# Optimization experiments

Hardware: AMD Instinct MI355X
Metric: run time of the kernel (lower is better)

## Reference

```python
import jax, jax.numpy as jnp
import numpy as np

W = 128
POS_FREQ = 10  # -> 3*10*2 = 60 encoded dims
VIEW_FREQ = 4  # -> 3*4*2 = 24 encoded dims


def freq_encode(v, n_freq):
    # tcnn 'Frequency' encoding: sin/cos of 2^j * pi * x per input dim.
    scales = (2.0 ** jnp.arange(n_freq, dtype=v.dtype)) * jnp.pi  # [F]
    ang = v[..., :, None] * scales  # [N, 3, F]
    enc = jnp.stack([jnp.sin(ang), jnp.cos(ang)], axis=-1)  # [N, 3, F, 2]
    return enc.reshape(v.shape[0], -1)  # [N, 3*F*2]


def mlp(h, weights):
    # tcnn FullyFusedMLP: bias-free, ReLU on hidden layers, linear output.
    for Wm in weights[:-1]:
        h = jax.nn.relu(h @ Wm)
    return h @ weights[-1]


def setup_inputs():
    key = jax.random.key(0)
    ks = jax.random.split(key, 10)
    N = 1048576

    def w(k, fan_in, fan_out):
        s = (1.0 / np.sqrt(fan_in)).astype(np.float32)
        return jax.random.uniform(k, (fan_in, fan_out), jnp.float32, -s, s)

    return {
        "x": jax.random.uniform(ks[0], (N, 6), jnp.float32),
        "Wd1_0": w(ks[1], 60, W),
        "Wd1_1": w(ks[2], W, W),
        "Wd1_2": w(ks[3], W, W),
        "Wd2_0": w(ks[4], 60 + W, W),
        "Wd2_1": w(ks[5], W, W),
        "Wd2_2": w(ks[6], W, W),
        "Wd2_3": w(ks[7], W, W + 1),
        "Wc_0": w(ks[8], 24 + W, W),
        "Wc_1": w(ks[9], W, 3),
    }


def reference(x, Wd1_0, Wd1_1, Wd1_2, Wd2_0, Wd2_1, Wd2_2, Wd2_3, Wc_0, Wc_1):
    pos, view = x[:, :3], x[:, 3:6]
    # Density MLP
    enc_pos = freq_encode(pos, POS_FREQ)                # [N, 60]
    part1 = mlp(enc_pos, [Wd1_0, Wd1_1, Wd1_2])          # [N, 128]
    dens_out = mlp(jnp.concatenate([enc_pos, part1], -1),
                   [Wd2_0, Wd2_1, Wd2_2, Wd2_3])         # [N, 129]
    blending = jax.nn.sigmoid(dens_out[:, :1])           # [N, 1]
    feature = dens_out[:, 1:]                            # [N, 128]
    density = feature[:, 0:1]                            # [N, 1]
    # Color MLP
    enc_view = freq_encode(view, VIEW_FREQ)              # [N, 24]
    rgb = mlp(jnp.concatenate([enc_view, feature], -1), [Wc_0, Wc_1])  # [N, 3]
    return jnp.concatenate([rgb, density, blending], -1)  # [N, 5]
```

## Files before the change

kernel.cpp:

```cpp
#include <hip/hip_runtime.h>
#include <cstdint>
#include <cstddef>

typedef __attribute__((ext_vector_type(8))) __bf16 bf16x8;
typedef __attribute__((ext_vector_type(16))) float floatx16;

struct SrcPtrs { const float* p[9]; };


__global__ void prep_zero(unsigned short* __restrict__ ws) {
  uint4* p = (uint4*)ws;
  const int n = 143360 / 8;
  for (int i = blockIdx.x * blockDim.x + threadIdx.x; i < n; i += gridDim.x * blockDim.x)
    p[i] = make_uint4(0u, 0u, 0u, 0u);
}

__global__ void prep_fill(SrcPtrs sp, unsigned short* __restrict__ ws) {
  const int m  = blockIdx.x >> 4;
  const int sl = blockIdx.x & 15;
  const int K[9]  = {60, 128, 128, 188, 128, 128, 128, 152, 128};
  const int N[9]  = {128, 128, 128, 128, 128, 128, 129, 128, 3};
  const int SS[9] = {4, 8, 8, 12, 8, 8, 8, 10, 8};
  const unsigned OFF[9] = {0u, 8192u, 24576u, 40960u, 65536u, 81920u, 98304u, 118784u, 139264u};
  const int Km = K[m], Nm = N[m], Sm = SS[m];
  const float* __restrict__ src = sp.p[m];
  unsigned short* __restrict__ dst = ws + OFF[m];
  const int tot = Km * Nm;
  for (int i = sl * 256 + (int)threadIdx.x; i < tot; i += 16 * 256) {
    int k = i / Nm;
    int n = i - k * Nm;
    int kk = k, row = n;
    if (m == 3) kk = (k < 60) ? 128 + k : k - 60;
    if (m == 7) kk = (k < 24) ? 128 + k : k - 24;
    if (m == 6) row = (n == 0) ? 128 : n - 1;
    kk = (kk & ~12) | (((kk & 4) << 1) | ((kk & 8) >> 1));
    const int t = row >> 5, l31 = row & 31;
    const int s = kk >> 4, q2 = (kk >> 3) & 1, j = kk & 7;
    dst[(t * Sm + s) * 512 + (q2 * 32 + l31) * 8 + j] =
        __builtin_bit_cast(unsigned short, (__bf16)src[i]);
  }
}


__device__ __forceinline__ unsigned pk2(float a, float b) {
  unsigned short ua = __builtin_bit_cast(unsigned short, (__bf16)a);
  unsigned short ub = __builtin_bit_cast(unsigned short, (__bf16)b);
  return (unsigned)ua | ((unsigned)ub << 16);
}

__device__ __forceinline__ void stage16(const void* g, void* l) {
  __builtin_amdgcn_global_load_lds(
      (const __attribute__((address_space(1))) unsigned int*)g,
      (__attribute__((address_space(3))) unsigned int*)l, 16, 0, 0);
}

template <int KIND>
__device__ __forceinline__ bf16x8 trig_frag(const float (&x)[6], int q2, int sl) {
  bf16x8 r;
#pragma unroll
  for (int j = 0; j < 8; ++j) {
    const int kA = 16 * sl + j + (j >= 4 ? 4 : 0);
    const int kB = kA + 4;
    int dA, dB; float scA, scB; bool vA, vB;
    if (KIND == 0) {
      vA = kA < 60; vB = kB < 60;
      dA = kA / 20; dB = kB / 20;
      scA = (float)(1 << ((kA % 20) >> 1)) * 0.5f;
      scB = (float)(1 << ((kB % 20) >> 1)) * 0.5f;
    } else {
      vA = kA < 24; vB = kB < 24;
      dA = 3 + (kA >> 3); dB = 3 + (kB >> 3);
      scA = (float)(1 << ((kA & 7) >> 1)) * 0.5f;
      scB = (float)(1 << ((kB & 7) >> 1)) * 0.5f;
    }
    float v  = q2 ? x[dB] : x[dA];
    float sc = q2 ? scB : scA;
    bool ok  = q2 ? vB : vA;
    float rev = v * sc;
    float t = (j & 1) ? __builtin_amdgcn_cosf(rev) : __builtin_amdgcn_sinf(rev);
    r[j] = (__bf16)(ok ? t : 0.0f);
  }
  return r;
}

template <bool RELU, int OUTM>
__device__ __forceinline__ void store_tile(int t, const floatx16& am0, const floatx16& am1,
                                           uint4 (&pout)[2][8], float* __restrict__ out,
                                           int q2, int pt0, int pt1) {
  if (OUTM == 2) {
    if (q2 == 0) {
      float* o0 = out + (size_t)pt0 * 5;
      o0[0] = am0[0]; o0[1] = am0[1]; o0[2] = am0[2];
      float* o1 = out + (size_t)pt1 * 5;
      o1[0] = am1[0]; o1[1] = am1[1]; o1[2] = am1[2];
    }
  } else {
    if (OUTM == 0 || t < 4) {
#pragma unroll
      for (int gg = 0; gg < 4; ++gg) {
        float b0 = am0[4 * gg], b1 = am0[4 * gg + 1];
        float b2 = am0[4 * gg + 2], b3 = am0[4 * gg + 3];
        float c0 = am1[4 * gg], c1 = am1[4 * gg + 1];
        float c2 = am1[4 * gg + 2], c3 = am1[4 * gg + 3];
        if (RELU) {
          b0 = fmaxf(b0, 0.f); b1 = fmaxf(b1, 0.f);
          b2 = fmaxf(b2, 0.f); b3 = fmaxf(b3, 0.f);
          c0 = fmaxf(c0, 0.f); c1 = fmaxf(c1, 0.f);
          c2 = fmaxf(c2, 0.f); c3 = fmaxf(c3, 0.f);
        }
        if ((gg & 1) == 0) {
          pout[0][2 * t + (gg >> 1)].x = pk2(b0, b1);
          pout[0][2 * t + (gg >> 1)].y = pk2(b2, b3);
          pout[1][2 * t + (gg >> 1)].x = pk2(c0, c1);
          pout[1][2 * t + (gg >> 1)].y = pk2(c2, c3);
        } else {
          pout[0][2 * t + (gg >> 1)].z = pk2(b0, b1);
          pout[0][2 * t + (gg >> 1)].w = pk2(b2, b3);
          pout[1][2 * t + (gg >> 1)].z = pk2(c0, c1);
          pout[1][2 * t + (gg >> 1)].w = pk2(c2, c3);
        }
      }
    }
    if (OUTM == 1 && q2 == 0) {
      if (t == 0) {
        out[(size_t)pt0 * 5 + 3] = am0[0];
        out[(size_t)pt1 * 5 + 3] = am1[0];
      }
      if (t == 4) {
        out[(size_t)pt0 * 5 + 4] = 1.0f / (1.0f + __expf(-am0[0]));
        out[(size_t)pt1 * 5 + 4] = 1.0f / (1.0f + __expf(-am1[0]));
      }
    }
  }
}

template <int S, int SL, int NT, int HT, int PP, bool RELU, int OUTM, int NB>
__device__ __forceinline__ void run_layer(const unsigned short* __restrict__ wsrc,
                                          const unsigned short* __restrict__ nsrc,
                                          unsigned short* __restrict__ sWt,
                                          const uint4 (&pin)[2][8],
                                          uint4 (&pout)[2][8],
                                          const bf16x8 (&tail)[2][4],
                                          float* __restrict__ out, int base, int tid) {
  const int lane = tid & 63;
  const int w = tid >> 6;
  const int q2 = lane >> 5;
  const int l31 = lane & 31;
  const int pt0 = base + w * 64 + l31;
  const int pt1 = pt0 + 32;

  __syncthreads();

  if (NB > 0) {
    const uint4* __restrict__ s4 = (const uint4*)nsrc;
    uint4* __restrict__ dst = (uint4*)(sWt + (PP ^ 1) * 12288);
#pragma unroll
    for (int kI = 0; kI < NB / (16 * 256); ++kI) {
      const int i = kI * 256 + tid;
      stage16(s4 + i, dst + (i & ~63));
    }
  }

  const unsigned short* __restrict__ ldsbuf = sWt + PP * 12288;
  const uint4* __restrict__ wp = (const uint4*)wsrc;

#pragma unroll
  for (int tp = 0; tp < NT / 2; ++tp) {
    const int t0 = 2 * tp, t1 = 2 * tp + 1;
    floatx16 a00, a01, a10, a11;
#pragma unroll
    for (int i = 0; i < 16; ++i) { a00[i] = 0.f; a01[i] = 0.f; a10[i] = 0.f; a11[i] = 0.f; }
    __builtin_amdgcn_s_setprio(1);
#pragma unroll
    for (int s = 0; s < S; ++s) {
      bf16x8 A0, A1;
      if (t0 < HT) A0 = *(const bf16x8*)&ldsbuf[(t0 * S + s) * 512 + lane * 8];
      else         A0 = __builtin_bit_cast(bf16x8, wp[(t0 * S + s) * 64 + lane]);
      if (t1 < HT) A1 = *(const bf16x8*)&ldsbuf[(t1 * S + s) * 512 + lane * 8];
      else         A1 = __builtin_bit_cast(bf16x8, wp[(t1 * S + s) * 64 + lane]);
      bf16x8 B0 = (s < SL) ? __builtin_bit_cast(bf16x8, pin[0][(s < SL) ? s : 0])
                           : tail[0][s - SL];
      bf16x8 B1 = (s < SL) ? __builtin_bit_cast(bf16x8, pin[1][(s < SL) ? s : 0])
                           : tail[1][s - SL];
      a00 = __builtin_amdgcn_mfma_f32_32x32x16_bf16(A0, B0, a00, 0, 0, 0);
      a01 = __builtin_amdgcn_mfma_f32_32x32x16_bf16(A0, B1, a01, 0, 0, 0);
      a10 = __builtin_amdgcn_mfma_f32_32x32x16_bf16(A1, B0, a10, 0, 0, 0);
      a11 = __builtin_amdgcn_mfma_f32_32x32x16_bf16(A1, B1, a11, 0, 0, 0);
    }
    __builtin_amdgcn_s_setprio(0);
    store_tile<RELU, OUTM>(t0, a00, a01, pout, out, q2, pt0, pt1);
    store_tile<RELU, OUTM>(t1, a10, a11, pout, out, q2, pt0, pt1);
  }

  if (NT & 1) {
    const int t = NT - 1;
    floatx16 a0, a1;
#pragma unroll
    for (int i = 0; i < 16; ++i) { a0[i] = 0.f; a1[i] = 0.f; }
    __builtin_amdgcn_s_setprio(1);
#pragma unroll
    for (int s = 0; s < S; ++s) {
      bf16x8 A;
      if (t < HT) A = *(const bf16x8*)&ldsbuf[(t * S + s) * 512 + lane * 8];
      else        A = __builtin_bit_cast(bf16x8, wp[(t * S + s) * 64 + lane]);
      bf16x8 B0 = (s < SL) ? __builtin_bit_cast(bf16x8, pin[0][(s < SL) ? s : 0])
                           : tail[0][s - SL];
      bf16x8 B1 = (s < SL) ? __builtin_bit_cast(bf16x8, pin[1][(s < SL) ? s : 0])
                           : tail[1][s - SL];
      a0 = __builtin_amdgcn_mfma_f32_32x32x16_bf16(A, B0, a0, 0, 0, 0);
      a1 = __builtin_amdgcn_mfma_f32_32x32x16_bf16(A, B1, a1, 0, 0, 0);
    }
    __builtin_amdgcn_s_setprio(0);
    store_tile<RELU, OUTM>(t, a0, a1, pout, out, q2, pt0, pt1);
  }
}

__global__ __launch_bounds__(256, 2) void nerf_main(const float* __restrict__ x,
                                                    const unsigned short* __restrict__ ws,
                                                    float* __restrict__ out) {
  __shared__ __align__(16) unsigned short sWt[2 * 12288];

  const int tid = (int)threadIdx.x;
  const int base = (int)blockIdx.x * 256;
  const int lane = tid & 63;
  const int w = tid >> 6;
  const int q2 = lane >> 5;
  const int l31 = lane & 31;
  const int pt0 = base + w * 64 + l31;

  {
    const uint4* s4 = (const uint4*)ws;
    uint4* dst = (uint4*)sWt;
#pragma unroll
    for (int i = 0; i < 2; ++i)
      stage16(s4 + i * 256 + tid, dst + ((i * 256 + tid) & ~63));
  }

  float x0[6], x1[6];
  {
    const float* a = x + (size_t)pt0 * 6;
    const float* b = x + (size_t)(pt0 + 32) * 6;
#pragma unroll
    for (int c = 0; c < 3; ++c) {
      float2 u = *(const float2*)(a + 2 * c);
      float2 v = *(const float2*)(b + 2 * c);
      x0[2 * c] = u.x; x0[2 * c + 1] = u.y;
      x1[2 * c] = v.x; x1[2 * c + 1] = v.y;
    }
  }

  bf16x8 pkt[2][4];
#pragma unroll
  for (int sl = 0; sl < 4; ++sl) {
    pkt[0][sl] = trig_frag<0>(x0, q2, sl);
    pkt[1][sl] = trig_frag<0>(x1, q2, sl);
  }

  uint4 P0[2][8], P1[2][8];

  run_layer< 4, 0, 4, 2, 0, true , 0, 16384>(ws + 0u,      ws + 8192u,   sWt, P0, P0, pkt, out, base, tid);
  run_layer< 8, 8, 4, 2, 1, true , 0, 16384>(ws + 8192u,   ws + 24576u,  sWt, P0, P1, pkt, out, base, tid);
  run_layer< 8, 8, 4, 2, 0, false, 0, 24576>(ws + 24576u,  ws + 40960u,  sWt, P1, P0, pkt, out, base, tid);
  run_layer<12, 8, 4, 2, 1, true , 0, 16384>(ws + 40960u,  ws + 65536u,  sWt, P0, P1, pkt, out, base, tid);
  run_layer< 8, 8, 4, 2, 0, true , 0, 16384>(ws + 65536u,  ws + 81920u,  sWt, P1, P0, pkt, out, base, tid);
  run_layer< 8, 8, 4, 2, 1, true , 0, 24576>(ws + 81920u,  ws + 98304u,  sWt, P0, P1, pkt, out, base, tid);
  run_layer< 8, 8, 5, 3, 0, false, 1, 20480>(ws + 98304u,  ws + 118784u, sWt, P1, P0, pkt, out, base, tid);

  bf16x8 vw[2][4];
#pragma unroll
  for (int sl = 0; sl < 2; ++sl) {
    vw[0][sl] = trig_frag<1>(x0, q2, sl);
    vw[1][sl] = trig_frag<1>(x1, q2, sl);
  }
  vw[0][2] = vw[0][0]; vw[0][3] = vw[0][0];
  vw[1][2] = vw[1][0]; vw[1][3] = vw[1][0];

  run_layer<10, 8, 4, 2, 1, true , 0,  8192>(ws + 118784u, ws + 139264u, sWt, P0, P1, vw,  out, base, tid);
  run_layer< 8, 8, 1, 1, 0, false, 2,     0>(ws + 139264u, (const unsigned short*)nullptr, sWt, P1, P0, pkt, out, base, tid);
}

extern "C" void kernel_launch(void* const* d_in, const int* in_sizes, int n_in,
                              void* d_out, int out_size, void* d_ws, size_t ws_size,
                              hipStream_t stream) {
  (void)n_in; (void)out_size; (void)ws_size;
  const float* x = (const float*)d_in[0];
  SrcPtrs sp;
  for (int i = 0; i < 9; ++i) sp.p[i] = (const float*)d_in[1 + i];
  unsigned short* ws = (unsigned short*)d_ws;
  float* out = (float*)d_out;
  const int N = in_sizes[0] / 6;

  prep_zero<<<70, 256, 0, stream>>>(ws);
  prep_fill<<<144, 256, 0, stream>>>(sp, ws);
  nerf_main<<<N / 256, 256, 0, stream>>>(x, ws, out);
}
```

Baseline: 339.0 us.

## Software-pipeline weight fragment loads with sliding window, process one tile at a time

Replaces the paired-tile MFMA loop with a flattened loop over all (tile, k-step) pairs. A 6-deep register window prefetches weight fragments from LDS or global ahead of use, and each tile starts from a shared zero accumulator instead of a per-tile zero fill. The aim is to hide load latency and cut accumulator register pressure. In exchange it drops the two-tile interleaving, so consecutive MFMAs depend on each other more often, and it removes the setprio hints.

```diff
diff --git a/kernel.cpp b/kernel.cpp
--- a/kernel.cpp
+++ b/kernel.cpp
@@ -141,6 +141,7 @@
                                           const uint4 (&pin)[2][8],
                                           uint4 (&pout)[2][8],
                                           const bf16x8 (&tail)[2][4],
+                                          floatx16 ZACC,
                                           float* __restrict__ out, int base, int tid) {
   const int lane = tid & 63;
   const int w = tid >> 6;
@@ -164,54 +165,38 @@
   const unsigned short* __restrict__ ldsbuf = sWt + PP * 12288;
   const uint4* __restrict__ wp = (const uint4*)wsrc;
 
-#pragma unroll
-  for (int tp = 0; tp < NT / 2; ++tp) {
-    const int t0 = 2 * tp, t1 = 2 * tp + 1;
-    floatx16 a00, a01, a10, a11;
-#pragma unroll
-    for (int i = 0; i < 16; ++i) { a00[i] = 0.f; a01[i] = 0.f; a10[i] = 0.f; a11[i] = 0.f; }
-    __builtin_amdgcn_s_setprio(1);
-#pragma unroll
-    for (int s = 0; s < S; ++s) {
-      bf16x8 A0, A1;
-      if (t0 < HT) A0 = *(const bf16x8*)&ldsbuf[(t0 * S + s) * 512 + lane * 8];
-      else         A0 = __builtin_bit_cast(bf16x8, wp[(t0 * S + s) * 64 + lane]);
-      if (t1 < HT) A1 = *(const bf16x8*)&ldsbuf[(t1 * S + s) * 512 + lane * 8];
-      else         A1 = __builtin_bit_cast(bf16x8, wp[(t1 * S + s) * 64 + lane]);
-      bf16x8 B0 = (s < SL) ? __builtin_bit_cast(bf16x8, pin[0][(s < SL) ? s : 0])
-                           : tail[0][s - SL];
-      bf16x8 B1 = (s < SL) ? __builtin_bit_cast(bf16x8, pin[1][(s < SL) ? s : 0])
-                           : tail[1][s - SL];
-      a00 = __builtin_amdgcn_mfma_f32_32x32x16_bf16(A0, B0, a00, 0, 0, 0);
-      a01 = __builtin_amdgcn_mfma_f32_32x32x16_bf16(A0, B1, a01, 0, 0, 0);
-      a10 = __builtin_amdgcn_mfma_f32_32x32x16_bf16(A1, B0, a10, 0, 0, 0);
-      a11 = __builtin_amdgcn_mfma_f32_32x32x16_bf16(A1, B1, a11, 0, 0, 0);
-    }
-    __builtin_amdgcn_s_setprio(0);
-    store_tile<RELU, OUTM>(t0, a00, a01, pout, out, q2, pt0, pt1);
-    store_tile<RELU, OUTM>(t1, a10, a11, pout, out, q2, pt0, pt1);
-  }
-
-  if (NT & 1) {
-    const int t = NT - 1;
-    floatx16 a0, a1;
-#pragma unroll
-    for (int i = 0; i < 16; ++i) { a0[i] = 0.f; a1[i] = 0.f; }
-    __builtin_amdgcn_s_setprio(1);
-#pragma unroll
-    for (int s = 0; s < S; ++s) {
-      bf16x8 A;
-      if (t < HT) A = *(const bf16x8*)&ldsbuf[(t * S + s) * 512 + lane * 8];
-      else        A = __builtin_bit_cast(bf16x8, wp[(t * S + s) * 64 + lane]);
-      bf16x8 B0 = (s < SL) ? __builtin_bit_cast(bf16x8, pin[0][(s < SL) ? s : 0])
-                           : tail[0][s - SL];
-      bf16x8 B1 = (s < SL) ? __builtin_bit_cast(bf16x8, pin[1][(s < SL) ? s : 0])
-                           : tail[1][s - SL];
+  auto loadA = [&](int p) -> bf16x8 {
+    const int t = p / S, s = p % S;
+    if (t < HT) return *(const bf16x8*)&ldsbuf[(t * S + s) * 512 + lane * 8];
+    return __builtin_bit_cast(bf16x8, wp[(t * S + s) * 64 + lane]);
+  };
+
+  constexpr int TOT = NT * S;
+  constexpr int DEPTH = 6;
+  bf16x8 win[DEPTH];
+
+#pragma unroll
+  for (int p = 0; p < DEPTH && p < TOT; ++p) win[p] = loadA(p);
+
+  floatx16 a0, a1;
+#pragma unroll
+  for (int p = 0; p < TOT; ++p) {
+    const int t = p / S, s = p % S;
+    bf16x8 A = win[p % DEPTH];
+    if (p + DEPTH < TOT) win[p % DEPTH] = loadA(p + DEPTH);
+    bf16x8 B0 = (s < SL) ? __builtin_bit_cast(bf16x8, pin[0][(s < SL) ? s : 0])
+                         : tail[0][s - SL];
+    bf16x8 B1 = (s < SL) ? __builtin_bit_cast(bf16x8, pin[1][(s < SL) ? s : 0])
+                         : tail[1][s - SL];
+    if (s == 0) {
+      a0 = __builtin_amdgcn_mfma_f32_32x32x16_bf16(A, B0, ZACC, 0, 0, 0);
+      a1 = __builtin_amdgcn_mfma_f32_32x32x16_bf16(A, B1, ZACC, 0, 0, 0);
+    } else {
       a0 = __builtin_amdgcn_mfma_f32_32x32x16_bf16(A, B0, a0, 0, 0, 0);
       a1 = __builtin_amdgcn_mfma_f32_32x32x16_bf16(A, B1, a1, 0, 0, 0);
     }
-    __builtin_amdgcn_s_setprio(0);
-    store_tile<RELU, OUTM>(t, a0, a1, pout, out, q2, pt0, pt1);
+    if (s == S - 1)
+      store_tile<RELU, OUTM>(t, a0, a1, pout, out, q2, pt0, pt1);
   }
 }
 
@@ -256,15 +241,19 @@
     pkt[1][sl] = trig_frag<0>(x1, q2, sl);
   }
 
+  floatx16 zacc;
+#pragma unroll
+  for (int i = 0; i < 16; ++i) zacc[i] = 0.0f;
+
   uint4 P0[2][8], P1[2][8];
 
-  run_layer< 4, 0, 4, 2, 0, true , 0, 16384>(ws + 0u,      ws + 8192u,   sWt, P0, P0, pkt, out, base, tid);
-  run_layer< 8, 8, 4, 2, 1, true , 0, 16384>(ws + 8192u,   ws + 24576u,  sWt, P0, P1, pkt, out, base, tid);
-  run_layer< 8, 8, 4, 2, 0, false, 0, 24576>(ws + 24576u,  ws + 40960u,  sWt, P1, P0, pkt, out, base, tid);
-  run_layer<12, 8, 4, 2, 1, true , 0, 16384>(ws + 40960u,  ws + 65536u,  sWt, P0, P1, pkt, out, base, tid);
-  run_layer< 8, 8, 4, 2, 0, true , 0, 16384>(ws + 65536u,  ws + 81920u,  sWt, P1, P0, pkt, out, base, tid);
-  run_layer< 8, 8, 4, 2, 1, true , 0, 24576>(ws + 81920u,  ws + 98304u,  sWt, P0, P1, pkt, out, base, tid);
-  run_layer< 8, 8, 5, 3, 0, false, 1, 20480>(ws + 98304u,  ws + 118784u, sWt, P1, P0, pkt, out, base, tid);
+  run_layer< 4, 0, 4, 2, 0, true , 0, 16384>(ws + 0u,      ws + 8192u,   sWt, P0, P0, pkt, zacc, out, base, tid);
+  run_layer< 8, 8, 4, 2, 1, true , 0, 16384>(ws + 8192u,   ws + 24576u,  sWt, P0, P1, pkt, zacc, out, base, tid);
+  run_layer< 8, 8, 4, 2, 0, false, 0, 24576>(ws + 24576u,  ws + 40960u,  sWt, P1, P0, pkt, zacc, out, base, tid);
+  run_layer<12, 8, 4, 2, 1, true , 0, 16384>(ws + 40960u,  ws + 65536u,  sWt, P0, P1, pkt, zacc, out, base, tid);
+  run_layer< 8, 8, 4, 2, 0, true , 0, 16384>(ws + 65536u,  ws + 81920u,  sWt, P1, P0, pkt, zacc, out, base, tid);
+  run_layer< 8, 8, 4, 2, 1, true , 0, 24576>(ws + 81920u,  ws + 98304u,  sWt, P0, P1, pkt, zacc, out, base, tid);
+  run_layer< 8, 8, 5, 3, 0, false, 1, 20480>(ws + 98304u,  ws + 118784u, sWt, P1, P0, pkt, zacc, out, base, tid);
 
   bf16x8 vw[2][4];
 #pragma unroll
@@ -275,8 +264,8 @@
   vw[0][2] = vw[0][0]; vw[0][3] = vw[0][0];
   vw[1][2] = vw[1][0]; vw[1][3] = vw[1][0];
 
-  run_layer<10, 8, 4, 2, 1, true , 0,  8192>(ws + 118784u, ws + 139264u, sWt, P0, P1, vw,  out, base, tid);
-  run_layer< 8, 8, 1, 1, 0, false, 2,     0>(ws + 139264u, (const unsigned short*)nullptr, sWt, P1, P0, pkt, out, base, tid);
+  run_layer<10, 8, 4, 2, 1, true , 0,  8192>(ws + 118784u, ws + 139264u, sWt, P0, P1, vw,  zacc, out, base, tid);
+  run_layer< 8, 8, 1, 1, 0, false, 2,     0>(ws + 139264u, (const unsigned short*)nullptr, sWt, P1, P0, pkt, zacc, out, base, tid);
 }
 
 extern "C" void kernel_launch(void* const* d_in, const int* in_sizes, int n_in,
```

Measured after the change: 349.5 us. 3.1% more time.
